# Optimization experiments

Measured on AMD Instinct MI355X. Metric: run time of the kernel, lower is better.

Reference implementation:

```python
import math
import jax, jax.numpy as jnp
from jax import lax
import numpy as np

B, CIN, COUT, K, SD, NCLS, H, W = 8, 512, 512, 3, 512, 35, 64, 64
EPS_DEMOD = 1e-8
EPS_IN = 1e-5  # torch InstanceNorm2d default eps


def _equal_linear(x, w, b):
    # EqualLinear: F.linear(x, w * (1/sqrt(in_dim))) + b  (lr_mul=1)
    return x @ (w.T * (1.0 / math.sqrt(w.shape[1]))) + b


def setup_inputs() -> dict:
    key = jax.random.key(0)
    ks = jax.random.split(key, 8)
    return {
        "input": jax.random.normal(ks[0], (B, CIN, H, W), jnp.float32),
        "style": jax.random.normal(ks[1], (B, SD), jnp.float32),
        "class_style": jax.random.normal(ks[2], (NCLS, SD), jnp.float32),
        "weight": jax.random.normal(ks[3], (1, COUT, CIN, K, K), jnp.float32),
        "mod_w": jax.random.normal(ks[4], (CIN, SD), jnp.float32),
        "mod_b": jnp.ones((CIN,), jnp.float32),  # bias_init=1
        "cw_w": jax.random.normal(ks[5], (COUT, SD), jnp.float32),
        "cw_b": jnp.ones((COUT,), jnp.float32),
        "cb_w": jax.random.normal(ks[6], (COUT, SD), jnp.float32),
        "cb_b": jnp.ones((COUT,), jnp.float32),
        "label_class_dict": jax.random.randint(ks[7], (B, H, W), 0, NCLS),
    }


def reference(input, style, class_style, weight, mod_w, mod_b, cw_w, cw_b, cb_w, cb_b, label_class_dict):
    scale = 1.0 / math.sqrt(CIN * K * K)
    pad = K // 2

    # per-sample style modulation of weights
    s = _equal_linear(style, mod_w, mod_b)                 # [B, CIN]
    w = scale * weight * s[:, None, :, None, None]         # [B, COUT, CIN, K, K]
    demod = lax.rsqrt(jnp.sum(w * w, axis=(2, 3, 4)) + EPS_DEMOD)  # [B, COUT]
    w = w * demod[:, :, None, None, None]

    # grouped conv (groups = batch) == vmap of per-sample conv
    def conv_one(x, wb):  # x [CIN,H,W], wb [COUT,CIN,K,K]
        return lax.conv_general_dilated(
            x[None], wb, window_strides=(1, 1), padding=[(pad, pad), (pad, pad)],
            dimension_numbers=("NCHW", "OIHW", "NCHW"))[0]

    out = jax.vmap(conv_one)(input, w)                     # [B, COUT, H, W]

    # param-free instance norm (biased variance, no affine)
    mu = out.mean(axis=(2, 3), keepdims=True)
    var = out.var(axis=(2, 3), keepdims=True)
    out = (out - mu) * lax.rsqrt(var + EPS_IN)

    # CLADE per-class affine from class_style, gathered via label map
    cw = _equal_linear(class_style, cw_w, cw_b)            # [NCLS, COUT]
    cb = _equal_linear(class_style, cb_w, cb_b)            # [NCLS, COUT]
    class_weight = jnp.transpose(cw[label_class_dict], (0, 3, 1, 2))  # [B,COUT,H,W]
    class_bias = jnp.transpose(cb[label_class_dict], (0, 3, 1, 2))
    return out * class_weight + class_bias
```

## Files before the change

kernel.cpp:

```cpp
#include <hip/hip_runtime.h>

typedef unsigned short u16;
typedef unsigned int u32;
typedef __attribute__((ext_vector_type(8))) short short8;
typedef __attribute__((ext_vector_type(4))) float floatx4;

typedef const u32 __attribute__((address_space(1))) glb_u32;
typedef u32 __attribute__((address_space(3))) lds_u32;

__device__ inline float bf2f(u16 h) {
  union { u32 u; float f; } v; v.u = ((u32)h) << 16; return v.f;
}
__device__ inline u16 f2bf(float f) {
  union { float f; u32 u; } v; v.f = f;
  u32 u = v.u;
  return (u16)((u + 0x7fffu + ((u >> 16) & 1u)) >> 16);
}
__device__ inline float ldf(const void* p, int i, int isbf) {
  return isbf ? bf2f(((const u16*)p)[i]) : ((const float*)p)[i];
}
__device__ inline void gl16(const void* g, void* l) {
  __builtin_amdgcn_global_load_lds((glb_u32*)g, (lds_u32*)l, 16, 0, 0);
}

__global__ __launch_bounds__(256) void prep_kernel(
    const void* __restrict__ style, const void* __restrict__ class_style,
    const void* __restrict__ weight,
    const void* __restrict__ mod_w, const void* __restrict__ mod_b,
    const void* __restrict__ cw_w, const void* __restrict__ cw_b,
    const void* __restrict__ cb_w, const void* __restrict__ cb_b,
    const void* __restrict__ x,
    float* __restrict__ s, float* __restrict__ cw, float* __restrict__ cb,
    u16* __restrict__ wT, float* __restrict__ wsqT2, u16* __restrict__ xT) {
  __shared__ float smem[4608];
  __shared__ int cnt;
  const int t = threadIdx.x;

  if (t == 0) cnt = 0;
  __syncthreads();
  {
    u32 v = ((const u32*)weight)[1024 + t];
    int e = (v >> 7) & 0xFF;
    if (e >= 96 && e <= 160) atomicAdd(&cnt, 1);
  }
  __syncthreads();
  const int isbf = (cnt >= 154) ? 1 : 0;
  const int bid = blockIdx.x;

  if (bid < 78) {
    int row = bid;
    const void *vec, *wm, *bias; float* out; int voff;
    if (row < 8)        { vec = style;       voff = row*512;      wm = mod_w; bias = mod_b; out = s  + row*512; }
    else if (row < 43)  { vec = class_style; voff = (row-8)*512;  wm = cw_w;  bias = cw_b;  out = cw + (row-8)*512; }
    else                { vec = class_style; voff = (row-43)*512; wm = cb_w;  bias = cb_b;  out = cb + (row-43)*512; }
    float* v = smem;
    for (int i = t; i < 512; i += 256) v[i] = ldf(vec, voff + i, isbf);
    __syncthreads();
    const float inv = 0.04419417382415922f;
    for (int o = t; o < 512; o += 256) {
      float acc = 0.f;
      if (isbf) {
        for (int k = 0; k < 512; ++k) acc += bf2f(((const u16*)wm)[o*512 + k]) * v[k];
      } else {
        const float4* wr = (const float4*)((const float*)wm + o*512);
        for (int k = 0; k < 128; ++k) {
          float4 p = wr[k];
          acc += p.x*v[k*4+0] + p.y*v[k*4+1] + p.z*v[k*4+2] + p.w*v[k*4+3];
        }
      }
      out[o] = acc * inv + ldf(bias, o, isbf);
    }
  } else if (bid < 590) {
    const int co = bid - 78;
    const int ctb = co >> 6, col = co & 63;
    float* wsmem = smem;
    for (int i = t; i < 4608; i += 256)
      wsmem[i] = ldf(weight, co*4608 + i, isbf);
    __syncthreads();
    for (int ci = t; ci < 512; ci += 256) {
      float sq = 0.f;
      const int ck = ci >> 5, q = (ci >> 3) & 3, e = ci & 7;
      #pragma unroll
      for (int tap = 0; tap < 9; ++tap) {
        float fv = wsmem[ci*9 + tap];
        sq += fv*fv;
        wT[((size_t)(ck*8 + ctb)*2304 + (tap*4 + q)*64 + col)*8 + e] = f2bf(fv);
      }
      wsqT2[(size_t)co*512 + ci] = sq;
    }
  } else {
    const int r = bid - 590;
    const int h8 = r & 7, ck = (r >> 3) & 15, b = r >> 7;
    float* sv = smem;
    float* pr = smem + 512;
    float* sl = smem + 768;
    for (int i = t; i < 512; i += 256) sv[i] = ldf(style, b*512 + i, isbf);
    __syncthreads();
    const float inv = 0.04419417382415922f;
    {
      const int row = t >> 3, seg = t & 7;
      const int ci = ck*32 + row;
      const float* svp = sv + seg*64;
      float partial = 0.f;
      if (isbf) {
        const u16* wr = (const u16*)mod_w + (size_t)ci*512 + seg*64;
        #pragma unroll
        for (int k = 0; k < 64; ++k) partial += bf2f(wr[k]) * svp[k];
      } else {
        const float4* wr = (const float4*)((const float*)mod_w + (size_t)ci*512 + seg*64);
        #pragma unroll
        for (int k = 0; k < 16; ++k) {
          float4 p = wr[k];
          partial += p.x*svp[k*4+0] + p.y*svp[k*4+1] + p.z*svp[k*4+2] + p.w*svp[k*4+3];
        }
      }
      pr[t] = partial;
    }
    __syncthreads();
    if (t < 32) {
      float a = 0.f;
      #pragma unroll
      for (int g = 0; g < 8; ++g) a += pr[t*8 + g];
      sl[t] = a * inv + ldf(mod_b, ck*32 + t, isbf);
    }
    __syncthreads();
    const int w = t & 63, cq = t >> 6;
    float sreg[8];
    #pragma unroll
    for (int j = 0; j < 8; ++j) sreg[j] = sl[cq*8 + j];
    for (int hh = 0; hh < 8; ++hh) {
      const int h = h8*8 + hh;
      float f[8];
      #pragma unroll
      for (int j = 0; j < 8; ++j) {
        float xv = ldf(x, (((b*512) + ck*32 + cq*8 + j)*64 + h)*64 + w, isbf);
        f[j] = xv * sreg[j];
      }
      u32 outp[4];
      #pragma unroll
      for (int i = 0; i < 4; ++i)
        outp[i] = (u32)f2bf(f[2*i]) | ((u32)f2bf(f[2*i+1]) << 16);
      uint4 po = {outp[0], outp[1], outp[2], outp[3]};
      *(uint4*)&xT[((size_t)(((b*16 + ck)*64 + h)*256) + t)*8] = po;
    }
  }
}

__global__ __launch_bounds__(512, 2) void conv_kernel(const u16* __restrict__ xT, const u16* __restrict__ wT,
                                                      float* __restrict__ y, float* __restrict__ part) {
  __shared__ __align__(16) u16 xs[18*4*67*8];
  __shared__ __align__(16) u16 wsm[2*2304*8];
  const int tid = threadIdx.x;
  const int lane = tid & 63;
  const int wid = tid >> 6;
  const int bid = blockIdx.x;
  const int b = bid & 7, ctb = (bid >> 3) & 7, hb = bid >> 6;
  const int ct0 = ctb * 64;
  const int h0 = hb * 16;
  const int m = lane & 15, qd = lane >> 4;

  {
    uint4 z = {0,0,0,0};
    for (int i = tid; i < 4824; i += 512) *(uint4*)&xs[i*8] = z;
  }

  floatx4 acc[4][8];
  #pragma unroll
  for (int i = 0; i < 4; ++i) {
    #pragma unroll
    for (int j = 0; j < 8; ++j) acc[i][j] = (floatx4)(0.f);
  }

  #define STAGE_X(ckn)                                                                     \
    for (int sl = wid; sl < 72; sl += 8) {                                                 \
      int dr = sl >> 2, q = sl & 3;                                                        \
      int hin = h0 + dr - 1;                                                               \
      if (hin >= 0 && hin <= 63) {                                                         \
        const u16* src = xT + ((size_t)(((b*16 + (ckn))*64 + hin)*256 + q*64 + lane))*8;   \
        gl16(src, &xs[((dr*4 + q)*67 + 1)*8]);                                             \
      }                                                                                    \
    }
  #define STAGE_W(ckn, bn)                                                                 \
    for (int j = wid; j < 36; j += 8) {                                                    \
      const u16* src = wT + ((size_t)(((ckn)*8 + ctb)*2304 + j*64 + lane))*8;              \
      gl16(src, &wsm[((bn)*2304 + j*64)*8]);                                               \
    }

  __syncthreads();
  STAGE_W(0, 0);

  for (int ck = 0; ck < 16; ++ck) {
    const int buf = ck & 1;
    __syncthreads();

    STAGE_X(ck);
    asm volatile("s_waitcnt vmcnt(0)" ::: "memory");
    __syncthreads();

    if (ck < 15) STAGE_W(ck + 1, buf ^ 1);

    const u16* wb = &wsm[buf*2304*8];
    #pragma unroll
    for (int tap = 0; tap < 9; ++tap) {
      const int k1 = tap / 3, k2 = tap - k1*3;
      short8 af[4], bfr[8];
      #pragma unroll
      for (int mi = 0; mi < 4; ++mi)
        af[mi] = *(const short8*)&wb[((tap*4 + qd)*64 + mi*16 + m)*8];
      #pragma unroll
      for (int hh = 0; hh < 2; ++hh) {
        const int dr = wid*2 + hh + k1;
        #pragma unroll
        for (int nw = 0; nw < 4; ++nw)
          bfr[hh*4 + nw] = *(const short8*)&xs[((dr*4 + qd)*67 + nw*16 + m + k2)*8];
      }
      #pragma unroll
      for (int ni = 0; ni < 8; ++ni) {
        #pragma unroll
        for (int mi = 0; mi < 4; ++mi)
          acc[mi][ni] = __builtin_amdgcn_mfma_f32_16x16x32_bf16(af[mi], bfr[ni], acc[mi][ni], 0, 0, 0);
      }
    }
  }
  #undef STAGE_X
  #undef STAGE_W

  #pragma unroll
  for (int mi = 0; mi < 4; ++mi) {
    #pragma unroll
    for (int hh = 0; hh < 2; ++hh) {
      const int h = h0 + wid*2 + hh;
      #pragma unroll
      for (int nw = 0; nw < 4; ++nw) {
        #pragma unroll
        for (int r = 0; r < 4; ++r) {
          int co = ct0 + mi*16 + qd*4 + r;
          int w = nw*16 + m;
          y[(size_t)(((b*512) + co)*64 + h)*64 + w] = acc[mi][hh*4 + nw][r];
        }
      }
    }
  }

  float s1[16], s2[16];
  #pragma unroll
  for (int mi = 0; mi < 4; ++mi) {
    #pragma unroll
    for (int r = 0; r < 4; ++r) {
      float a = 0.f, aa = 0.f;
      #pragma unroll
      for (int ni = 0; ni < 8; ++ni) {
        float v = acc[mi][ni][r];
        a += v; aa += v*v;
      }
      s1[mi*4+r] = a; s2[mi*4+r] = aa;
    }
  }
  #pragma unroll
  for (int off = 1; off < 16; off <<= 1) {
    #pragma unroll
    for (int i = 0; i < 16; ++i) {
      s1[i] += __shfl_xor(s1[i], off, 64);
      s2[i] += __shfl_xor(s2[i], off, 64);
    }
  }
  __syncthreads();
  float* red = (float*)xs;
  if (m == 0) {
    #pragma unroll
    for (int mi = 0; mi < 4; ++mi) {
      #pragma unroll
      for (int r = 0; r < 4; ++r) {
        int co = mi*16 + qd*4 + r;
        red[(wid*64 + co)*2 + 0] = s1[mi*4+r];
        red[(wid*64 + co)*2 + 1] = s2[mi*4+r];
      }
    }
  }
  __syncthreads();
  if (tid < 128) {
    int co = tid >> 1, which = tid & 1;
    float v = 0.f;
    #pragma unroll
    for (int w8 = 0; w8 < 8; ++w8) v += red[(w8*64 + co)*2 + which];
    part[(size_t)(((b*4 + hb)*512) + ct0 + co)*2 + which] = v;
  }
}

__global__ __launch_bounds__(256) void epi_kernel(float* __restrict__ y, const float* __restrict__ part,
                                                  const float* __restrict__ s, const float* __restrict__ wsqT2,
                                                  const float* __restrict__ cw, const float* __restrict__ cb,
                                                  const int* __restrict__ label) {
  const int bc = blockIdx.x;
  const int b = bc >> 9, co = bc & 511;
  const int t = threadIdx.x;
  __shared__ float tabw[35], tabb[35];
  __shared__ float redp[4];
  __shared__ float2 msh;
  if (t < 35) { tabw[t] = cw[t*512 + co]; tabb[t] = cb[t*512 + co]; }

  const float* sb = s + b*512;
  const float* wq = wsqT2 + (size_t)co*512;
  float ep;
  {
    float s0 = sb[t], s1v = sb[t + 256];
    ep = s0*s0*wq[t] + s1v*s1v*wq[t + 256];
  }
  #pragma unroll
  for (int off = 1; off < 64; off <<= 1) ep += __shfl_xor(ep, off, 64);
  if ((t & 63) == 0) redp[t >> 6] = ep;
  __syncthreads();
  if (t == 0) {
    float SS = redp[0] + redp[1] + redp[2] + redp[3];
    float S = 0.f, Q = 0.f;
    const float2* pv = (const float2*)part;
    #pragma unroll
    for (int hb = 0; hb < 4; ++hb) {
      float2 p = pv[(size_t)((b*4 + hb)*512) + co];
      S += p.x; Q += p.y;
    }
    float mval = S * (1.f/4096.f);
    float var = fmaxf(Q * (1.f/4096.f) - mval*mval, 0.f);
    float eps = 1e-5f*SS + 4.608e-10f;
    msh = make_float2(mval, rsqrtf(var + eps));
  }
  __syncthreads();
  const float mval = msh.x, is = msh.y;

  float* yp = y + (size_t)bc*4096 + t*16;
  const int* lp = label + b*4096 + t*16;
  #pragma unroll
  for (int u = 0; u < 4; ++u) {
    float4 v = *(const float4*)(yp + u*4);
    int4 l = *(const int4*)(lp + u*4);
    float4 o;
    o.x = (v.x - mval)*is*tabw[l.x] + tabb[l.x];
    o.y = (v.y - mval)*is*tabw[l.y] + tabb[l.y];
    o.z = (v.z - mval)*is*tabw[l.z] + tabb[l.z];
    o.w = (v.w - mval)*is*tabw[l.w] + tabb[l.w];
    *(float4*)(yp + u*4) = o;
  }
}

extern "C" void kernel_launch(void* const* d_in, const int* in_sizes, int n_in,
                              void* d_out, int out_size, void* d_ws, size_t ws_size,
                              hipStream_t stream) {
  (void)in_sizes; (void)n_in; (void)out_size; (void)ws_size;
  const void* input       = d_in[0];
  const void* style       = d_in[1];
  const void* class_style = d_in[2];
  const void* weight      = d_in[3];
  const void* mod_w       = d_in[4];
  const void* mod_b       = d_in[5];
  const void* cw_w        = d_in[6];
  const void* cw_b        = d_in[7];
  const void* cb_w        = d_in[8];
  const void* cb_b        = d_in[9];
  const int* label        = (const int*)d_in[10];
  float* y = (float*)d_out;

  char* ws = (char*)d_ws;
  u16*   xT    = (u16*)  (ws + 0);
  u16*   wT    = (u16*)  (ws + 33554432);
  float* wsqT2 = (float*)(ws + 38273024);
  float* s     = (float*)(ws + 39321600);
  float* cw    = (float*)(ws + 39337984);
  float* cb    = (float*)(ws + 39409664);
  float* part  = (float*)(ws + 39481344);

  hipLaunchKernelGGL(prep_kernel, dim3(1614), dim3(256), 0, stream,
                     style, class_style, weight, mod_w, mod_b, cw_w, cw_b, cb_w, cb_b,
                     input, s, cw, cb, wT, wsqT2, xT);
  hipLaunchKernelGGL(conv_kernel, dim3(256), dim3(512), 0, stream, xT, wT, y, part);
  hipLaunchKernelGGL(epi_kernel, dim3(4096), dim3(256), 0, stream, y, part, s, wsqT2, cw, cb, label);
}
```

Baseline: 320.6 us.

## Fuse instance-norm and CLADE epilogue into conv via inter-block spin barrier

The conv kernel now applies the normalization and per-class affine directly to its accumulators. Each group of four row-blocks sharing a batch and channel tile synchronizes through a global atomic counter with a spin-wait, then reads the combined partial statistics. This removes the separate epilogue kernel and its full read-modify-write of the output tensor. It relies on all 256 blocks being co-resident, which is checked with an occupancy query before taking the fused path. It also adds a transposed weight-square table in prep and extra global stores there.

```diff
diff --git a/kernel.cpp b/kernel.cpp
--- a/kernel.cpp
+++ b/kernel.cpp
@@ -31,10 +31,14 @@
     const void* __restrict__ cb_w, const void* __restrict__ cb_b,
     const void* __restrict__ x,
     float* __restrict__ s, float* __restrict__ cw, float* __restrict__ cb,
-    u16* __restrict__ wT, float* __restrict__ wsqT2, u16* __restrict__ xT) {
+    u16* __restrict__ wT, float* __restrict__ wsqT2, float* __restrict__ wsqT1,
+    u16* __restrict__ xT, int* __restrict__ bar) {
   __shared__ float smem[4608];
   __shared__ int cnt;
   const int t = threadIdx.x;
+  const int bid = blockIdx.x;
+
+  if (bid == 0 && t < 64) bar[t] = 0;
 
   if (t == 0) cnt = 0;
   __syncthreads();
@@ -45,7 +49,6 @@
   }
   __syncthreads();
   const int isbf = (cnt >= 154) ? 1 : 0;
-  const int bid = blockIdx.x;
 
   if (bid < 78) {
     int row = bid;
@@ -87,6 +90,7 @@
         wT[((size_t)(ck*8 + ctb)*2304 + (tap*4 + q)*64 + col)*8 + e] = f2bf(fv);
       }
       wsqT2[(size_t)co*512 + ci] = sq;
+      wsqT1[(size_t)ci*512 + co] = sq;
     }
   } else {
     const int r = bid - 590;
@@ -146,8 +150,12 @@
   }
 }
 
-__global__ __launch_bounds__(512, 2) void conv_kernel(const u16* __restrict__ xT, const u16* __restrict__ wT,
-                                                      float* __restrict__ y, float* __restrict__ part) {
+template<int FUSED>
+__global__ __launch_bounds__(512, 2) void conv_t(const u16* __restrict__ xT, const u16* __restrict__ wT,
+                                                 float* __restrict__ y, float* __restrict__ part,
+                                                 const float* __restrict__ s, const float* __restrict__ wsqT1,
+                                                 const float* __restrict__ cw, const float* __restrict__ cb,
+                                                 const int* __restrict__ label, int* __restrict__ bar) {
   __shared__ __align__(16) u16 xs[18*4*67*8];
   __shared__ __align__(16) u16 wsm[2*2304*8];
   const int tid = threadIdx.x;
@@ -225,18 +233,20 @@
   #undef STAGE_X
   #undef STAGE_W
 
-  #pragma unroll
-  for (int mi = 0; mi < 4; ++mi) {
-    #pragma unroll
-    for (int hh = 0; hh < 2; ++hh) {
-      const int h = h0 + wid*2 + hh;
-      #pragma unroll
-      for (int nw = 0; nw < 4; ++nw) {
-        #pragma unroll
-        for (int r = 0; r < 4; ++r) {
-          int co = ct0 + mi*16 + qd*4 + r;
-          int w = nw*16 + m;
-          y[(size_t)(((b*512) + co)*64 + h)*64 + w] = acc[mi][hh*4 + nw][r];
+  if constexpr (!FUSED) {
+    #pragma unroll
+    for (int mi = 0; mi < 4; ++mi) {
+      #pragma unroll
+      for (int hh = 0; hh < 2; ++hh) {
+        const int h = h0 + wid*2 + hh;
+        #pragma unroll
+        for (int nw = 0; nw < 4; ++nw) {
+          #pragma unroll
+          for (int r = 0; r < 4; ++r) {
+            int co = ct0 + mi*16 + qd*4 + r;
+            int w = nw*16 + m;
+            y[(size_t)(((b*512) + co)*64 + h)*64 + w] = acc[mi][hh*4 + nw][r];
+          }
         }
       }
     }
@@ -284,6 +294,93 @@
     #pragma unroll
     for (int w8 = 0; w8 < 8; ++w8) v += red[(w8*64 + co)*2 + which];
     part[(size_t)(((b*4 + hb)*512) + ct0 + co)*2 + which] = v;
+  }
+
+  if constexpr (FUSED) {
+    const int g = b*8 + ctb;
+    __threadfence();
+    __syncthreads();
+    if (tid == 0) atomicAdd(&bar[g], 1);
+
+    char* xbase = (char*)xs;
+    float2* tab  = (float2*)(xbase + 4096);
+    int*    labs = (int*)  (xbase + 22592);
+    float*  epred= (float*)(xbase + 26688);
+    float2* ms   = (float2*)(xbase + 28736);
+
+    for (int i = tid; i < 2240; i += 512) {
+      int cls = i >> 6, col = i & 63;
+      tab[cls*66 + col] = make_float2(cw[cls*512 + ct0 + col], cb[cls*512 + ct0 + col]);
+    }
+    for (int i = tid; i < 1024; i += 512)
+      labs[i] = label[(b*64 + h0 + (i >> 6))*64 + (i & 63)];
+    {
+      const int col = tid & 63, seg = tid >> 6;
+      const float* sb = s + b*512 + seg*64;
+      const float* wq = wsqT1 + (size_t)(seg*64)*512 + ct0 + col;
+      float ep = 0.f;
+      #pragma unroll 8
+      for (int k = 0; k < 64; ++k) {
+        float sv = sb[k];
+        ep += sv*sv * wq[(size_t)k*512];
+      }
+      epred[tid] = ep;
+    }
+    __syncthreads();
+
+    if (tid == 0) {
+      while (__hip_atomic_load(&bar[g], __ATOMIC_RELAXED, __HIP_MEMORY_SCOPE_AGENT) < 4)
+        __builtin_amdgcn_s_sleep(2);
+    }
+    __syncthreads();
+    __threadfence();
+
+    if (tid < 64) {
+      float S = 0.f, Q = 0.f;
+      const float2* pv = (const float2*)part;
+      #pragma unroll
+      for (int hbb = 0; hbb < 4; ++hbb) {
+        float2 p = pv[(size_t)((b*4 + hbb)*512) + ct0 + tid];
+        S += p.x; Q += p.y;
+      }
+      float SS = 0.f;
+      #pragma unroll
+      for (int sg = 0; sg < 8; ++sg) SS += epred[sg*64 + tid];
+      float mval = S * (1.f/4096.f);
+      float var = fmaxf(Q * (1.f/4096.f) - mval*mval, 0.f);
+      float eps = 1e-5f*SS + 4.608e-10f;
+      ms[tid] = make_float2(mval, rsqrtf(var + eps));
+    }
+    __syncthreads();
+
+    float2 msv[4][4];
+    #pragma unroll
+    for (int mi = 0; mi < 4; ++mi) {
+      #pragma unroll
+      for (int r = 0; r < 4; ++r) msv[mi][r] = ms[mi*16 + qd*4 + r];
+    }
+    #pragma unroll
+    for (int hh = 0; hh < 2; ++hh) {
+      const int h = h0 + wid*2 + hh;
+      #pragma unroll
+      for (int nw = 0; nw < 4; ++nw) {
+        const int w = nw*16 + m;
+        const float2* trow = tab + labs[(wid*2 + hh)*64 + w]*66 + qd*4;
+        #pragma unroll
+        for (int mi = 0; mi < 4; ++mi) {
+          float4 p0 = *(const float4*)&trow[mi*16];
+          float4 p2 = *(const float4*)&trow[mi*16 + 2];
+          float wxv[4] = {p0.x, p0.z, p2.x, p2.z};
+          float wyv[4] = {p0.y, p0.w, p2.y, p2.w};
+          float* yp = &y[(size_t)(((b*512) + ct0 + mi*16 + qd*4)*64 + h)*64 + w];
+          #pragma unroll
+          for (int r = 0; r < 4; ++r) {
+            float a = (acc[mi][hh*4 + nw][r] - msv[mi][r].x) * msv[mi][r].y;
+            yp[(size_t)r*4096] = a*wxv[r] + wyv[r];
+          }
+        }
+      }
+    }
   }
 }
 
@@ -367,10 +464,29 @@
   float* cw    = (float*)(ws + 39337984);
   float* cb    = (float*)(ws + 39409664);
   float* part  = (float*)(ws + 39481344);
+  float* wsqT1 = (float*)(ws + 39612416);
+  int*   bar   = (int*)  (ws + 40660992);
 
   hipLaunchKernelGGL(prep_kernel, dim3(1614), dim3(256), 0, stream,
                      style, class_style, weight, mod_w, mod_b, cw_w, cw_b, cb_w, cb_b,
-                     input, s, cw, cb, wT, wsqT2, xT);
-  hipLaunchKernelGGL(conv_kernel, dim3(256), dim3(512), 0, stream, xT, wT, y, part);
-  hipLaunchKernelGGL(epi_kernel, dim3(4096), dim3(256), 0, stream, y, part, s, wsqT2, cw, cb, label);
-}
+                     input, s, cw, cb, wT, wsqT2, wsqT1, xT, bar);
+
+  static int fused_ok = -1;
+  if (fused_ok < 0) {
+    int nb = 0, ncu = 0, dev = 0;
+    hipError_t e1 = hipOccupancyMaxActiveBlocksPerMultiprocessor(&nb, conv_t<1>, 512, 0);
+    hipError_t e2 = hipGetDevice(&dev);
+    hipError_t e3 = hipDeviceGetAttribute(&ncu, hipDeviceAttributeMultiprocessorCount, dev);
+    fused_ok = (e1 == hipSuccess && e2 == hipSuccess && e3 == hipSuccess &&
+                nb >= 1 && (long)nb * (long)ncu >= 256) ? 1 : 0;
+  }
+
+  if (fused_ok) {
+    hipLaunchKernelGGL((conv_t<1>), dim3(256), dim3(512), 0, stream,
+                       xT, wT, y, part, s, wsqT1, cw, cb, label, bar);
+  } else {
+    hipLaunchKernelGGL((conv_t<0>), dim3(256), dim3(512), 0, stream,
+                       xT, wT, y, part, s, wsqT1, cw, cb, label, bar);
+    hipLaunchKernelGGL(epi_kernel, dim3(4096), dim3(256), 0, stream, y, part, s, wsqT2, cw, cb, label);
+  }
+}
```

Result: no change. 321.3 us (+0.2%).

## Double-buffer input tiles in LDS and read weights directly from global

Applied to the files above, without the earlier changes.

Drops the LDS weight buffer and uses the freed space to double-buffer the input halo tile. The next channel chunk is prefetched asynchronously with global_load_lds while MFMAs run on the current one. Out-of-range halo rows are redirected to a dummy slot so every wave has a fixed vmcnt to wait on. Weight fragments are now loaded from global memory (L1/L2) inside the tap loop. That removes weight staging but adds global-load latency right in front of the MFMA chain.

```diff
diff --git a/kernel.cpp b/kernel.cpp
--- a/kernel.cpp
+++ b/kernel.cpp
@@ -148,8 +148,7 @@
 
 __global__ __launch_bounds__(512, 2) void conv_kernel(const u16* __restrict__ xT, const u16* __restrict__ wT,
                                                       float* __restrict__ y, float* __restrict__ part) {
-  __shared__ __align__(16) u16 xs[18*4*67*8];
-  __shared__ __align__(16) u16 wsm[2*2304*8];
+  __shared__ __align__(16) u16 xs[(2*4824 + 64)*8];
   const int tid = threadIdx.x;
   const int lane = tid & 63;
   const int wid = tid >> 6;
@@ -161,7 +160,7 @@
 
   {
     uint4 z = {0,0,0,0};
-    for (int i = tid; i < 4824; i += 512) *(uint4*)&xs[i*8] = z;
+    for (int i = tid; i < 9648; i += 512) *(uint4*)&xs[i*8] = z;
   }
 
   floatx4 acc[4][8];
@@ -171,48 +170,50 @@
     for (int j = 0; j < 8; ++j) acc[i][j] = (floatx4)(0.f);
   }
 
-  #define STAGE_X(ckn)                                                                     \
-    for (int sl = wid; sl < 72; sl += 8) {                                                 \
-      int dr = sl >> 2, q = sl & 3;                                                        \
-      int hin = h0 + dr - 1;                                                               \
-      if (hin >= 0 && hin <= 63) {                                                         \
-        const u16* src = xT + ((size_t)(((b*16 + (ckn))*64 + hin)*256 + q*64 + lane))*8;   \
-        gl16(src, &xs[((dr*4 + q)*67 + 1)*8]);                                             \
+  #define STAGE_X(ckn, bn)                                                                 \
+    {                                                                                      \
+      u16* xb = &xs[(bn)*4824*8];                                                          \
+      u16* dum = &xs[9648*8];                                                              \
+      for (int sl = wid; sl < 72; sl += 8) {                                               \
+        int dr = sl >> 2, q = sl & 3;                                                      \
+        int hin = h0 + dr - 1;                                                             \
+        int valid = (hin >= 0 && hin <= 63);                                               \
+        const u16* src = xT + ((size_t)(((b*16 + (ckn))*64 + (valid ? hin : 0))*256        \
+                                        + q*64 + lane))*8;                                 \
+        gl16(src, valid ? &xb[((dr*4 + q)*67 + 1)*8] : dum);                               \
       }                                                                                    \
     }
-  #define STAGE_W(ckn, bn)                                                                 \
-    for (int j = wid; j < 36; j += 8) {                                                    \
-      const u16* src = wT + ((size_t)(((ckn)*8 + ctb)*2304 + j*64 + lane))*8;              \
-      gl16(src, &wsm[((bn)*2304 + j*64)*8]);                                               \
-    }
-
-  __syncthreads();
-  STAGE_W(0, 0);
+
+  __syncthreads();
+  STAGE_X(0, 0);
+  asm volatile("s_waitcnt vmcnt(0)" ::: "memory");
+  __syncthreads();
 
   for (int ck = 0; ck < 16; ++ck) {
     const int buf = ck & 1;
-    __syncthreads();
-
-    STAGE_X(ck);
-    asm volatile("s_waitcnt vmcnt(0)" ::: "memory");
-    __syncthreads();
-
-    if (ck < 15) STAGE_W(ck + 1, buf ^ 1);
-
-    const u16* wb = &wsm[buf*2304*8];
+    if (ck < 15) {
+      STAGE_X(ck + 1, buf ^ 1);
+      asm volatile("s_waitcnt vmcnt(9)" ::: "memory");
+    } else {
+      asm volatile("s_waitcnt vmcnt(0)" ::: "memory");
+    }
+    __syncthreads();
+
+    const u16* xb = &xs[buf*4824*8];
+    const u16* wtg = wT + ((size_t)(ck*8 + ctb))*2304*8;
     #pragma unroll
     for (int tap = 0; tap < 9; ++tap) {
       const int k1 = tap / 3, k2 = tap - k1*3;
       short8 af[4], bfr[8];
       #pragma unroll
       for (int mi = 0; mi < 4; ++mi)
-        af[mi] = *(const short8*)&wb[((tap*4 + qd)*64 + mi*16 + m)*8];
+        af[mi] = *(const short8*)&wtg[((tap*4 + qd)*64 + mi*16 + m)*8];
       #pragma unroll
       for (int hh = 0; hh < 2; ++hh) {
         const int dr = wid*2 + hh + k1;
         #pragma unroll
         for (int nw = 0; nw < 4; ++nw)
-          bfr[hh*4 + nw] = *(const short8*)&xs[((dr*4 + qd)*67 + nw*16 + m + k2)*8];
+          bfr[hh*4 + nw] = *(const short8*)&xb[((dr*4 + qd)*67 + nw*16 + m + k2)*8];
       }
       #pragma unroll
       for (int ni = 0; ni < 8; ++ni) {
@@ -221,9 +222,9 @@
           acc[mi][ni] = __builtin_amdgcn_mfma_f32_16x16x32_bf16(af[mi], bfr[ni], acc[mi][ni], 0, 0, 0);
       }
     }
+    __syncthreads();
   }
   #undef STAGE_X
-  #undef STAGE_W
 
   #pragma unroll
   for (int mi = 0; mi < 4; ++mi) {
@@ -264,7 +265,6 @@
       s2[i] += __shfl_xor(s2[i], off, 64);
     }
   }
-  __syncthreads();
   float* red = (float*)xs;
   if (m == 0) {
     #pragma unroll
```

Measured after the change: 323.9 us. Within noise of the previous version (+1.0%).
